# Kernel optimization log

Hardware: AMD Instinct MI355X
Metric: run time of the kernel (lower is better)

## Reference

```python
import jax, jax.numpy as jnp
import numpy as np

B, T, D, C = 2, 2048, 1024, 10
F = D // 2 + 1  # rfft bins; permutations act on frequency bins (perm_freq=True)


def setup_inputs() -> dict:
    key = jax.random.key(0)
    ks = jax.random.split(key, 6)
    s = 1.0 / np.sqrt(D)
    x = jax.random.normal(ks[0], (B, T, D), jnp.float32)
    Wq = jax.random.normal(ks[1], (D, D), jnp.float32) * s
    Wk = jax.random.normal(ks[2], (D, D), jnp.float32) * s
    Wv = jax.random.normal(ks[3], (D, D), jnp.float32) * s
    Wo = jax.random.normal(ks[4], (D, D), jnp.float32) * s
    # buffer: torch.randn(C, F).argsort(-1) -> random permutations of freq bins
    perms = jnp.argsort(jax.random.normal(ks[5], (C, F)), axis=-1)
    return {"x": x, "Wq": Wq, "Wk": Wk, "Wv": Wv, "Wo": Wo, "perms": perms}


def reference(x, Wq, Wk, Wv, Wo, perms):
    # linear projections (nn.Linear applies x @ W.T)
    q = x @ Wq.T
    k = x @ Wk.T
    v = x @ Wv.T
    # HRR bind/unbind in rfft frequency domain
    fq = jnp.fft.rfft(q, axis=-1)  # (B,T,F) complex
    fk = jnp.fft.rfft(k, axis=-1)
    fv = jnp.fft.rfft(v, axis=-1)
    # gather permuted redundant copies of freq bins: (B,T,C,F) -> (C,B,T,F)
    fkp = jnp.moveaxis(fk[..., perms], 2, 0)
    fqp = jnp.moveaxis(fq[..., perms], 2, 0)
    # causal associative memory: cumulative sum of key*value bindings over time
    kv = jnp.cumsum(fkp * fv[None], axis=-2)  # (C,B,T,F)
    # unbind with query (circular correlation = multiply by conj), mean copies
    r = jnp.mean(kv * jnp.conj(fqp), axis=0)  # (B,T,F)
    values_hat = jnp.fft.irfft(r, n=D, axis=-1)  # (B,T,D)
    return values_hat @ Wo.T
```

## Files before the change

kernel.cpp:

```cpp
#include <hip/hip_runtime.h>
#include <math.h>

#define B_   2
#define T_   2048
#define D_   1024
#define C_   10
#define F_   513
#define NTOK (B_ * T_)
#define LF   3078
#define LFP  3136
#define KP2  1056
#define NCH  128
#define TC   (T_ / NCH)

typedef unsigned short us16;
typedef __attribute__((ext_vector_type(8))) __bf16 bf16x8;
typedef __attribute__((ext_vector_type(4))) float  f32x4;

#define O_XBF    ((size_t)0)
#define O_PREP   ((size_t)8388608)
#define O_WT     (O_PREP)
#define O_WOBF   (O_PREP + 6291456)
#define O_TCS    (O_PREP + 8388608)
#define O_RCAT   (O_PREP)
#define O_SFB    (O_PREP + 10489856)
#define O_MALLB  (O_SFB + 2162688)
#define O_MOUTB  (O_MALLB + 6303744)
#define O_FALL   (O_MOUTB + 2162688)
#define O_SSCAN  (O_FALL + 25690112)

__device__ __forceinline__ us16 f2b(float f) {
    union { float f; unsigned u; } v; v.f = f;
    unsigned r = v.u + 0x7FFFu + ((v.u >> 16) & 1u);
    return (us16)(r >> 16);
}

__device__ __forceinline__ float2 b2f2(unsigned w) {
    union { unsigned u; float f; } a, b;
    a.u = (w & 0xffffu) << 16;
    b.u = w & 0xffff0000u;
    return make_float2(a.f, b.f);
}

__device__ __forceinline__ void gl_lds16(const us16* g, us16* l) {
    __builtin_amdgcn_global_load_lds(
        (const __attribute__((address_space(1))) unsigned*)g,
        (__attribute__((address_space(3))) unsigned*)l, 16, 0, 0);
}

__global__ __launch_bounds__(256)
void hrr_prep(const float* __restrict__ x,  const float* __restrict__ Wq,
              const float* __restrict__ Wk, const float* __restrict__ Wv,
              const float* __restrict__ Wo,
              us16* __restrict__ Xbf, us16* __restrict__ WT,
              us16* __restrict__ WoBf, us16* __restrict__ Tcs,
              us16* __restrict__ Sfb) {
    __shared__ float t[32][33];
    const int bid = blockIdx.x, tid = threadIdx.x;
    if (bid < 4096) {
        int i = bid * 256 + tid;
        float4 v = ((const float4*)x)[i];
        ushort4 o;
        o.x = f2b(v.x); o.y = f2b(v.y); o.z = f2b(v.z); o.w = f2b(v.w);
        ((ushort4*)Xbf)[i] = o;
    } else if (bid < 5120) {
        int i = (bid - 4096) * 256 + tid;
        float4 v = ((const float4*)Wo)[i];
        ushort4 o;
        o.x = f2b(v.x); o.y = f2b(v.y); o.z = f2b(v.z); o.w = f2b(v.w);
        ((ushort4*)WoBf)[i] = o;
    } else if (bid < 8192) {
        const int l  = bid - 5120;
        const int bz = l >> 10, l2 = l & 1023;
        const int bx = (l2 & 31) * 32, by = (l2 >> 5) * 32;
        const float* W = (bz == 0) ? Wq : (bz == 1) ? Wk : Wv;
        us16* O = WT + (size_t)bz * D_ * D_;
        const int tx = tid & 31, ty = tid >> 5;
#pragma unroll
        for (int i = 0; i < 32; i += 8)
            t[ty + i][tx] = W[(size_t)(by + ty + i) * D_ + bx + tx];
        __syncthreads();
#pragma unroll
        for (int i = 0; i < 32; i += 8)
            O[(size_t)(bx + ty + i) * D_ + by + tx] = f2b(t[tx][ty + i]);
    } else if (bid < 12296) {
        int idx = (bid - 8192) * 256 + tid;
        int r = idx >> 10, e = idx & 1023;
        int f = r >> 1;
        float ang = (float)((f * e) & 1023) * 6.135923151542565e-3f;
        Tcs[idx] = f2b((r & 1) ? -sinf(ang) : cosf(ang));
    } else {
        int idx = (bid - 12296) * 256 + tid;
        int r = idx >> 10, e = idx & 1023;
        float v = 0.f;
        if (r < 1026) {
            int f = r >> 1;
            float s = (f == 0 || f == 512) ? (1.0f / 1024.0f) : (2.0f / 1024.0f);
            float ang = (float)((f * e) & 1023) * 6.135923151542565e-3f;
            v = (r & 1) ? -s * sinf(ang) : s * cosf(ang);
        }
        Sfb[idx] = f2b(v);
    }
}

template <bool OUT_BF16>
__device__ __forceinline__ void gemm_core(
    const us16* __restrict__ A, const us16* __restrict__ B, void* __restrict__ Cv,
    int M, int N, int K, int lda, int ldb, int ldc, int Ncap,
    int bm, int bn, us16* smem) {
    us16* As = smem;
    us16* Bs = smem + 8192;

    const int tid  = threadIdx.x;
    const int lane = tid & 63;
    const int wave = tid >> 6;
    const int wm = (wave >> 1) * 64;
    const int wn = (wave & 1) * 64;

    const int r0    = tid >> 2;
    const int g_lds = tid & 3;
    const int g_src = g_lds ^ ((r0 >> 1) & 3);
    const int c4    = g_src * 8;

    int rA0 = bm + r0;      if (rA0 >= M) rA0 = M - 1;
    int rA1 = bm + 64 + r0; if (rA1 >= M) rA1 = M - 1;
    int rB0 = bn + r0;      if (rB0 >= N) rB0 = N - 1;
    int rB1 = bn + 64 + r0; if (rB1 >= N) rB1 = N - 1;
    const us16* pA0 = A + (size_t)rA0 * lda + c4;
    const us16* pA1 = A + (size_t)rA1 * lda + c4;
    const us16* pB0 = B + (size_t)rB0 * ldb + c4;
    const us16* pB1 = B + (size_t)rB1 * ldb + c4;

    f32x4 acc[4][4];
#pragma unroll
    for (int i = 0; i < 4; i++)
#pragma unroll
        for (int j = 0; j < 4; j++) acc[i][j] = (f32x4){0.f, 0.f, 0.f, 0.f};

    const int fr = lane & 15;
    const int gq = ((lane >> 4) ^ ((fr >> 1) & 3)) * 8;

    const int wb = wave * 512;
#define STAGE_TILE(buf, ko)                                  \
    do {                                                     \
        us16* a_ = As + (buf) * 4096 + wb;                   \
        us16* b_ = Bs + (buf) * 4096 + wb;                   \
        gl_lds16(pA0 + (ko), a_);                            \
        gl_lds16(pA1 + (ko), a_ + 2048);                     \
        gl_lds16(pB0 + (ko), b_);                            \
        gl_lds16(pB1 + (ko), b_ + 2048);                     \
    } while (0)

    STAGE_TILE(0, 0);
    __syncthreads();

    int cur = 0;
    for (int k0 = 0; k0 < K; k0 += 32) {
        const int kn = k0 + 32;
        if (kn < K) STAGE_TILE(cur ^ 1, kn);

        const us16* Ac = As + cur * 4096;
        const us16* Bc = Bs + cur * 4096;
        bf16x8 af[4], bfr[4];
#pragma unroll
        for (int i = 0; i < 4; i++)
            af[i] = *(const bf16x8*)(Ac + (wm + i * 16 + fr) * 32 + gq);
#pragma unroll
        for (int j = 0; j < 4; j++)
            bfr[j] = *(const bf16x8*)(Bc + (wn + j * 16 + fr) * 32 + gq);
#pragma unroll
        for (int i = 0; i < 4; i++)
#pragma unroll
            for (int j = 0; j < 4; j++)
                acc[i][j] = __builtin_amdgcn_mfma_f32_16x16x32_bf16(bfr[j], af[i], acc[i][j], 0, 0, 0);

        __syncthreads();
        cur ^= 1;
    }
#undef STAGE_TILE

    const int cl  = lane & 15;
    const int rq  = (lane >> 4) * 4;
    float* lbuf = (float*)smem;
#pragma unroll
    for (int p = 0; p < 4; ++p) {
        __syncthreads();
        if ((wave >> 1) == (p >> 1)) {
            const int ib = (p & 1) * 2;
#pragma unroll
            for (int ii = 0; ii < 2; ++ii) {
                const int rl = ii * 16 + cl;
#pragma unroll
                for (int j = 0; j < 4; ++j)
                    *(f32x4*)(lbuf + rl * 132 + wn + j * 16 + rq) = acc[ib + ii][j];
            }
        }
        __syncthreads();
        const int rbase = bm + p * 32;
        if (OUT_BF16) {
            us16* C = (us16*)Cv;
#pragma unroll
            for (int rr = 0; rr < 2; ++rr) {
                const int idx = rr * 2048 + tid * 8;
                const int row = idx >> 7, col = idx & 127;
                const int grow = rbase + row, gcol = bn + col;
                if (grow < M && gcol + 8 <= Ncap) {
                    const float* s = lbuf + row * 132 + col;
                    uint4 o;
                    o.x = (unsigned)f2b(s[0]) | ((unsigned)f2b(s[1]) << 16);
                    o.y = (unsigned)f2b(s[2]) | ((unsigned)f2b(s[3]) << 16);
                    o.z = (unsigned)f2b(s[4]) | ((unsigned)f2b(s[5]) << 16);
                    o.w = (unsigned)f2b(s[6]) | ((unsigned)f2b(s[7]) << 16);
                    *(uint4*)(C + (size_t)grow * ldc + gcol) = o;
                }
            }
        } else {
            float* C = (float*)Cv;
#pragma unroll
            for (int rr = 0; rr < 4; ++rr) {
                const int idx = rr * 1024 + tid * 4;
                const int row = idx >> 7, col = idx & 127;
                const int grow = rbase + row, gcol = bn + col;
                if (grow < M && gcol + 4 <= Ncap)
                    *(float4*)(C + (size_t)grow * ldc + gcol) =
                        *(const float4*)(lbuf + row * 132 + col);
            }
        }
    }
}

template <bool OUT_BF16>
__global__ __launch_bounds__(256, 3)
void hrr_gemm(const us16* __restrict__ A, const us16* __restrict__ B,
              void* __restrict__ C, int M, int N, int K,
              int lda, int ldb, int ldc, int Ncap, int swz) {
    __shared__ us16 smem[16384];
    int bx = blockIdx.x, by = blockIdx.y;
    if (swz) {
        const int gx = gridDim.x;
        const int id = bx + gx * by;
        const int q = (gx * gridDim.y) >> 3;
        const int nid = (id & 7) * q + (id >> 3);
        bx = nid % gx; by = nid / gx;
    }
    gemm_core<OUT_BF16>(A, B, C, M, N, K, lda, ldb, ldc, Ncap,
                        by * 128, bx * 128, smem);
}

__global__ __launch_bounds__(256, 3)
void hrr_gemm_builders(const us16* __restrict__ Tcs, const us16* __restrict__ WT,
                       us16* __restrict__ MallB, const us16* __restrict__ WoBf,
                       const us16* __restrict__ Sfb, us16* __restrict__ MoutB) {
    __shared__ us16 smem[16384];
    const int bm = blockIdx.y * 128, bn = blockIdx.x * 128;
    const int z = blockIdx.z;
    if (z < 3)
        gemm_core<true>(Tcs, WT + (size_t)z * D_ * D_,
                        MallB + (size_t)z * 1026 * 1024,
                        1026, 1024, 1024, 1024, 1024, 1024, 1024, bm, bn, smem);
    else
        gemm_core<true>(WoBf, Sfb, MoutB,
                        1024, KP2, 1024, 1024, 1024, KP2, KP2, bm, bn, smem);
}

__global__ __launch_bounds__(256, 4)
void hrr_scan_sums(const us16* __restrict__ Fall, const int* __restrict__ perms,
                   float* __restrict__ S) {
    const int n = blockIdx.x, b = blockIdx.y, half = blockIdx.z;
    const int tid = threadIdx.x;
    const int f0 = half * 256;
    const int VL = half ? 257 : 256;
    __shared__ float2 kc[F_], vc[257];

    float aR[2][C_], aI[2][C_];
    int gg[2][C_];
#pragma unroll
    for (int i = 0; i < 2; i++) {
        const int f = (i == 0) ? (f0 + tid) : 512;
        const bool act = (i == 0) || (half == 1 && tid == 0);
#pragma unroll
        for (int c = 0; c < C_; c++) {
            gg[i][c] = act ? perms[c * F_ + f] : 0;
            aR[i][c] = aI[i][c] = 0.f;
        }
    }

    for (int tl = 0; tl < TC; tl++) {
        const us16* row = Fall + (size_t)(b * T_ + n * TC + tl) * LFP;
        __syncthreads();
        for (int j = tid; j < F_; j += 256)
            kc[j] = b2f2(*(const unsigned*)(row + 1026 + 2 * j));
        for (int j = tid; j < VL; j += 256)
            vc[j] = b2f2(*(const unsigned*)(row + 2052 + 2 * (f0 + j)));
        __syncthreads();
#pragma unroll
        for (int i = 0; i < 2; i++) {
            const int lv = (i == 0) ? tid : 256;
            if (i == 0 || (half == 1 && tid == 0)) {
                float2 v = vc[lv];
#pragma unroll
                for (int c = 0; c < C_; c++) {
                    float2 k = kc[gg[i][c]];
                    aR[i][c] += k.x * v.x - k.y * v.y;
                    aI[i][c] += k.x * v.y + k.y * v.x;
                }
            }
        }
    }
#pragma unroll
    for (int i = 0; i < 2; i++) {
        const int f = (i == 0) ? (f0 + tid) : 512;
        if (i == 0 || (half == 1 && tid == 0)) {
#pragma unroll
            for (int c = 0; c < C_; c++) {
                size_t a = ((((size_t)c * B_ + b) * NCH + n) * F_ + f) * 2;
                S[a] = aR[i][c]; S[a + 1] = aI[i][c];
            }
        }
    }
}

__global__ void hrr_scan_prefix(float* __restrict__ S) {
    int tid = blockIdx.x * 256 + threadIdx.x;
    if (tid >= C_ * B_ * F_) return;
    int c = tid / (B_ * F_);
    int r = tid % (B_ * F_);
    int b = r / F_, f = r % F_;
    size_t base = (((size_t)c * B_ + b) * NCH) * F_ + f;
    float runR = 0.f, runI = 0.f;
    for (int n0 = 0; n0 < NCH; n0 += 8) {
        float tR[8], tI[8];
#pragma unroll
        for (int u = 0; u < 8; u++) {
            size_t a = (base + (size_t)(n0 + u) * F_) * 2;
            tR[u] = S[a]; tI[u] = S[a + 1];
        }
#pragma unroll
        for (int u = 0; u < 8; u++) {
            size_t a = (base + (size_t)(n0 + u) * F_) * 2;
            S[a] = runR; S[a + 1] = runI;
            runR += tR[u]; runI += tI[u];
        }
    }
}

__global__ __launch_bounds__(256, 4)
void hrr_scan_apply(const us16* __restrict__ Fall, const int* __restrict__ perms,
                    const float* __restrict__ S, us16* __restrict__ Rcat) {
    const int n = blockIdx.x, b = blockIdx.y, half = blockIdx.z;
    const int tid = threadIdx.x;
    const int f0 = half * 256;
    const int VL = half ? 257 : 256;
    __shared__ float2 qc[F_], kc[F_], vc[257];

    float kvR[2][C_], kvI[2][C_];
    int gg[2][C_];
#pragma unroll
    for (int i = 0; i < 2; i++) {
        const int f = (i == 0) ? (f0 + tid) : 512;
        const bool act = (i == 0) || (half == 1 && tid == 0);
#pragma unroll
        for (int c = 0; c < C_; c++) {
            gg[i][c] = act ? perms[c * F_ + f] : 0;
            if (act) {
                size_t a = ((((size_t)c * B_ + b) * NCH + n) * F_ + f) * 2;
                kvR[i][c] = S[a]; kvI[i][c] = S[a + 1];
            } else { kvR[i][c] = 0.f; kvI[i][c] = 0.f; }
        }
    }

    for (int tl = 0; tl < TC; tl++) {
        const int tt = b * T_ + n * TC + tl;
        const us16* row = Fall + (size_t)tt * LFP;
        __syncthreads();
        for (int j = tid; j < F_; j += 256) {
            qc[j] = b2f2(*(const unsigned*)(row + 2 * j));
            kc[j] = b2f2(*(const unsigned*)(row + 1026 + 2 * j));
        }
        for (int j = tid; j < VL; j += 256)
            vc[j] = b2f2(*(const unsigned*)(row + 2052 + 2 * (f0 + j)));
        __syncthreads();
        unsigned* out32 = (unsigned*)(Rcat + (size_t)tt * KP2);
#pragma unroll
        for (int i = 0; i < 2; i++) {
            const int f = (i == 0) ? (f0 + tid) : 512;
            const int lv = (i == 0) ? tid : 256;
            if (i == 0 || (half == 1 && tid == 0)) {
                float2 v = vc[lv];
                float accR = 0.f, accI = 0.f;
#pragma unroll
                for (int c = 0; c < C_; c++) {
                    int g = gg[i][c];
                    float2 k = kc[g];
                    float nR = kvR[i][c] + k.x * v.x - k.y * v.y;
                    float nI = kvI[i][c] + k.x * v.y + k.y * v.x;
                    kvR[i][c] = nR; kvI[i][c] = nI;
                    float2 q = qc[g];
                    accR += nR * q.x + nI * q.y;
                    accI += nI * q.x - nR * q.y;
                }
                out32[f] = (unsigned)f2b(accR * 0.1f)
                         | ((unsigned)f2b(accI * 0.1f) << 16);
            }
        }
        if (half == 0 && tid < 15)
            out32[513 + tid] = 0;
    }
}

extern "C" void kernel_launch(void* const* d_in, const int* in_sizes, int n_in,
                              void* d_out, int out_size, void* d_ws, size_t ws_size,
                              hipStream_t stream) {
    const float* x  = (const float*)d_in[0];
    const float* Wq = (const float*)d_in[1];
    const float* Wk = (const float*)d_in[2];
    const float* Wv = (const float*)d_in[3];
    const float* Wo = (const float*)d_in[4];
    const int* perms = (const int*)d_in[5];
    float* out = (float*)d_out;

    char* ws = (char*)d_ws;
    us16* Xbf   = (us16*)(ws + O_XBF);
    us16* WT    = (us16*)(ws + O_WT);
    us16* WoBf  = (us16*)(ws + O_WOBF);
    us16* Tcs   = (us16*)(ws + O_TCS);
    us16* Sfb   = (us16*)(ws + O_SFB);
    us16* MallB = (us16*)(ws + O_MALLB);
    us16* MoutB = (us16*)(ws + O_MOUTB);
    us16* Rcat  = (us16*)(ws + O_RCAT);
    us16* Fall  = (us16*)(ws + O_FALL);
    float* Ssc  = (float*)(ws + O_SSCAN);

    hrr_prep<<<16520, 256, 0, stream>>>(x, Wq, Wk, Wv, Wo, Xbf, WT, WoBf, Tcs, Sfb);

    hrr_gemm_builders<<<dim3(9, 9, 4), 256, 0, stream>>>(Tcs, WT, MallB, WoBf, Sfb, MoutB);

    hrr_gemm<true><<<dim3(25, 32), 256, 0, stream>>>(
        Xbf, MallB, Fall, NTOK, LF, 1024, 1024, 1024, LFP, LFP, 1);

    hrr_scan_sums<<<dim3(NCH, B_, 2), 256, 0, stream>>>(Fall, perms, Ssc);
    hrr_scan_prefix<<<(C_ * B_ * F_ + 255) / 256, 256, 0, stream>>>(Ssc);
    hrr_scan_apply<<<dim3(NCH, B_, 2), 256, 0, stream>>>(Fall, perms, Ssc, Rcat);

    hrr_gemm<false><<<dim3(8, 32), 256, 0, stream>>>(
        Rcat, MoutB, out, NTOK, D_, KP2, KP2, KP2, D_, D_, 1);
}
```

Baseline: 243.3 us.

## Add dedicated 256x256-tile double-buffered GEMM kernel for main projection

Replaces the generic 128-tile GEMM for the fused QKV+DFT projection with a specialized 512-thread kernel using 256x256 output tiles, double-buffered direct global-to-LDS loads with XOR swizzling, block-id remapping for cache locality, and MFMA priority hints. Larger tiles raise arithmetic intensity and cut global traffic, and the epilogue stages results through LDS for coalesced bf16 stores. Fewer blocks (208) on a 256-CU part may leave CUs idle and risk a tail effect, and the large LDS footprint limits occupancy.

```diff
diff --git a/kernel.cpp b/kernel.cpp
--- a/kernel.cpp
+++ b/kernel.cpp
@@ -263,6 +263,168 @@
                         1024, KP2, 1024, 1024, 1024, KP2, KP2, bm, bn, smem);
 }
 
+__global__ __launch_bounds__(512, 2)
+void hrr_gemm_main(const us16* __restrict__ A, const us16* __restrict__ B,
+                   us16* __restrict__ C) {
+    __shared__ us16 smem[65536];
+    us16* Asb = smem;
+    us16* Bsb = smem + 32768;
+
+    const int tid  = threadIdx.x;
+    const int lane = tid & 63;
+    const int wave = tid >> 6;
+
+    int id = blockIdx.x + 13 * blockIdx.y;
+    id = (id & 7) * 26 + (id >> 3);
+    const int bx = id % 13, by = id / 13;
+    const int bm = by * 256, bn = bx * 256;
+
+    const int srow = tid >> 3;
+    const int sgr  = (tid & 7) ^ (srow & 7);
+    const us16* gA[4];
+    const us16* gB[4];
+#pragma unroll
+    for (int g = 0; g < 4; ++g) {
+        int ra = bm + g * 64 + srow; if (ra > NTOK - 1) ra = NTOK - 1;
+        int rb = bn + g * 64 + srow; if (rb > LF - 1)   rb = LF - 1;
+        gA[g] = A + (size_t)ra * 1024 + sgr * 8;
+        gB[g] = B + (size_t)rb * 1024 + sgr * 8;
+    }
+
+    f32x4 acc[8][4];
+#pragma unroll
+    for (int i = 0; i < 8; i++)
+#pragma unroll
+        for (int j = 0; j < 4; j++) acc[i][j] = (f32x4){0.f, 0.f, 0.f, 0.f};
+
+    const int wmw = (wave >> 2) * 128;
+    const int wnw = (wave & 3) * 64;
+    const int fr  = lane & 15;
+    const int gr  = lane >> 4;
+    const int l7  = lane & 7;
+
+#define STAGE3(buf, ko)                                            \
+    do {                                                           \
+        us16* a_ = Asb + (buf) * 16384 + wave * 512;               \
+        us16* b_ = Bsb + (buf) * 16384 + wave * 512;               \
+        gl_lds16(gA[0] + (ko), a_);                                \
+        gl_lds16(gA[1] + (ko), a_ + 4096);                         \
+        gl_lds16(gA[2] + (ko), a_ + 8192);                         \
+        gl_lds16(gA[3] + (ko), a_ + 12288);                        \
+        gl_lds16(gB[0] + (ko), b_);                                \
+        gl_lds16(gB[1] + (ko), b_ + 4096);                         \
+        gl_lds16(gB[2] + (ko), b_ + 8192);                         \
+        gl_lds16(gB[3] + (ko), b_ + 12288);                        \
+    } while (0)
+
+#define RBAR                                                       \
+    do {                                                           \
+        asm volatile("" ::: "memory");                             \
+        __builtin_amdgcn_s_barrier();                              \
+        asm volatile("" ::: "memory");                             \
+    } while (0)
+
+#define LOAD_A(ih)                                                              \
+    do {                                                                        \
+        _Pragma("unroll")                                                       \
+        for (int i = 0; i < 4; ++i)                                             \
+            _Pragma("unroll")                                                   \
+            for (int ks = 0; ks < 2; ++ks)                                      \
+                af[i][ks] = *(const bf16x8*)(Ac +                               \
+                    (wmw + (ih) * 64 + i * 16 + fr) * 64 +                      \
+                    (((ks << 2) | gr) ^ l7) * 8);                               \
+    } while (0)
+
+#define LOAD_B(jh)                                                              \
+    do {                                                                        \
+        _Pragma("unroll")                                                       \
+        for (int j = 0; j < 2; ++j)                                             \
+            _Pragma("unroll")                                                   \
+            for (int ks = 0; ks < 2; ++ks)                                      \
+                bfr[j][ks] = *(const bf16x8*)(Bc +                              \
+                    (wnw + (jh) * 32 + j * 16 + fr) * 64 +                      \
+                    (((ks << 2) | gr) ^ l7) * 8);                               \
+    } while (0)
+
+#define MFMA_Q(ih, jh)                                                          \
+    do {                                                                        \
+        __builtin_amdgcn_s_setprio(1);                                          \
+        _Pragma("unroll")                                                       \
+        for (int i = 0; i < 4; ++i)                                             \
+            _Pragma("unroll")                                                   \
+            for (int j = 0; j < 2; ++j)                                         \
+                _Pragma("unroll")                                               \
+                for (int ks = 0; ks < 2; ++ks)                                  \
+                    acc[(ih) * 4 + i][(jh) * 2 + j] =                           \
+                        __builtin_amdgcn_mfma_f32_16x16x32_bf16(                \
+                            bfr[j][ks], af[i][ks],                              \
+                            acc[(ih) * 4 + i][(jh) * 2 + j], 0, 0, 0);          \
+        __builtin_amdgcn_s_setprio(0);                                          \
+    } while (0)
+
+    STAGE3(0, 0);
+    asm volatile("s_waitcnt vmcnt(0)" ::: "memory");
+    __builtin_amdgcn_s_barrier();
+    asm volatile("" ::: "memory");
+
+    int cur = 0;
+#pragma unroll 1
+    for (int t = 0; t < 16; ++t) {
+        if (t < 15) STAGE3(cur ^ 1, (t + 1) * 64);
+
+        const us16* Ac = Asb + cur * 16384;
+        const us16* Bc = Bsb + cur * 16384;
+        bf16x8 af[4][2], bfr[2][2];
+
+        LOAD_A(0); LOAD_B(0); MFMA_Q(0, 0); RBAR;
+        LOAD_B(1);            MFMA_Q(0, 1); RBAR;
+        LOAD_A(1);            MFMA_Q(1, 1); RBAR;
+        LOAD_B(0);            MFMA_Q(1, 0);
+        asm volatile("s_waitcnt vmcnt(0)" ::: "memory");
+        __builtin_amdgcn_s_barrier();
+        asm volatile("" ::: "memory");
+        cur ^= 1;
+    }
+#undef STAGE3
+#undef LOAD_A
+#undef LOAD_B
+#undef MFMA_Q
+#undef RBAR
+
+    __syncthreads();
+    float* lw = (float*)smem + wave * (32 * 68);
+    const int cl = lane & 15;
+    const int rq = (lane >> 4) * 4;
+#pragma unroll
+    for (int p = 0; p < 4; ++p) {
+#pragma unroll
+        for (int ii = 0; ii < 2; ++ii) {
+            const int ifr = p * 2 + ii;
+#pragma unroll
+            for (int j = 0; j < 4; ++j)
+                *(f32x4*)(lw + (ii * 16 + cl) * 68 + j * 16 + rq) = acc[ifr][j];
+        }
+        __syncthreads();
+#pragma unroll
+        for (int rr = 0; rr < 4; ++rr) {
+            const int idx = rr * 512 + lane * 8;
+            const int row = idx >> 6, col = idx & 63;
+            const int grow = bm + wmw + p * 32 + row;
+            const int gcol = bn + wnw + col;
+            if (gcol + 8 <= LFP) {
+                const float* s = lw + row * 68 + col;
+                uint4 o;
+                o.x = (unsigned)f2b(s[0]) | ((unsigned)f2b(s[1]) << 16);
+                o.y = (unsigned)f2b(s[2]) | ((unsigned)f2b(s[3]) << 16);
+                o.z = (unsigned)f2b(s[4]) | ((unsigned)f2b(s[5]) << 16);
+                o.w = (unsigned)f2b(s[6]) | ((unsigned)f2b(s[7]) << 16);
+                *(uint4*)(C + (size_t)grow * LFP + gcol) = o;
+            }
+        }
+        __syncthreads();
+    }
+}
+
 __global__ __launch_bounds__(256, 4)
 void hrr_scan_sums(const us16* __restrict__ Fall, const int* __restrict__ perms,
                    float* __restrict__ S) {
@@ -435,8 +597,7 @@
 
     hrr_gemm_builders<<<dim3(9, 9, 4), 256, 0, stream>>>(Tcs, WT, MallB, WoBf, Sfb, MoutB);
 
-    hrr_gemm<true><<<dim3(25, 32), 256, 0, stream>>>(
-        Xbf, MallB, Fall, NTOK, LF, 1024, 1024, 1024, LFP, LFP, 1);
+    hrr_gemm_main<<<dim3(13, 16), 512, 0, stream>>>(Xbf, MallB, Fall);
 
     hrr_scan_sums<<<dim3(NCH, B_, 2), 256, 0, stream>>>(Fall, perms, Ssc);
     hrr_scan_prefix<<<(C_ * B_ * F_ + 255) / 256, 256, 0, stream>>>(Ssc);
```

Result: faster. 237.7 us (-2.3%).
